# Performance work log

Hardware: AMD Instinct MI355X
Metric: run time of the kernel (lower is better)

The kernel has to match this reference:

```python
import jax, jax.numpy as jnp
import numpy as np
from jax import lax

DN = ('NCHW', 'OIHW', 'NCHW')
BN_EPS = 1e-5


def _avg_pool(x, k, stride):
    # PyTorch AvgPool2d with count_include_pad=True: divide by k*k always
    p = k // 2
    s = lax.reduce_window(x, 0.0, lax.add, (1, 1, k, k), (1, 1, stride, stride),
                          [(0, 0), (0, 0), (p, p), (p, p)])
    return s / float(k * k)


def setup_inputs() -> dict:
    key = jax.random.key(0)
    k0, k1, k2 = jax.random.split(key, 3)
    x = jax.random.normal(k0, (8, 3, 1024, 1024), jnp.float32)
    weight = jax.random.normal(k1, (1, 5), jnp.float32)          # nn.Parameter(1,5)
    conv_w = jax.random.normal(k2, (5, 3, 7, 7), jnp.float32) * 0.05
    bn_gamma = jnp.ones((5,), jnp.float32)
    bn_beta = jnp.zeros((5,), jnp.float32)
    bn_mean = jnp.zeros((5,), jnp.float32)
    bn_var = jnp.ones((5,), jnp.float32)
    return {"x": x, "weight": weight, "conv_w": conv_w,
            "bn_gamma": bn_gamma, "bn_beta": bn_beta,
            "bn_mean": bn_mean, "bn_var": bn_var}


def reference(x, weight, conv_w, bn_gamma, bn_beta, bn_mean, bn_var):
    # stage 1: 3x3 avgpool stride 2
    x = _avg_pool(x, 3, 2)                                  # [b,3,512,512]
    image_a = jnp.mean(x, axis=1, keepdims=True)            # [b,1,512,512]

    # attention branch: Conv(3->5,k7,s2,p3) + BN(eval) -> spatial mean -> tanh
    wa = lax.conv_general_dilated(x, conv_w, (2, 2), [(3, 3), (3, 3)],
                                  dimension_numbers=DN)     # [b,5,256,256]
    wa = (wa - bn_mean[None, :, None, None]) * (bn_gamma[None, :, None, None] /
          jnp.sqrt(bn_var[None, :, None, None] + BN_EPS)) + bn_beta[None, :, None, None]
    weight_att = jnp.tanh(jnp.mean(wa, axis=(2, 3)))        # [b,5]

    # Gaussian-Laplacian kernel from learned scalar GL
    GL = weight[0, 0]
    a1 = GL * 4.0
    a2 = -a1 / 8.0
    a3 = -a1 / 16.0
    ker = jnp.zeros((1, 1, 5, 5), jnp.float32)
    for r, c in [(0, 2), (1, 1), (1, 3), (2, 0), (2, 4), (3, 1), (3, 3), (4, 2)]:
        ker = ker.at[0, 0, r, c].set(a3)
    for r, c in [(1, 2), (2, 1), (2, 3), (3, 2)]:
        ker = ker.at[0, 0, r, c].set(a2)
    ker = ker.at[0, 0, 2, 2].set(a1)

    x_GL = lax.conv_general_dilated(image_a, ker, (1, 1), [(2, 2), (2, 2)],
                                    dimension_numbers=DN)   # [b,1,512,512]
    x_GL = jnp.abs(x_GL)
    x_GL = jnp.where(x_GL < 1e-6, 0.0, x_GL)                # zero tiny values (relu is no-op after abs)

    b, c, h, w = x_GL.shape
    t = x_GL.reshape(b, 1, h * w)                           # [b,1,N]
    x_GL_max = jnp.max(t, axis=-1)                          # [b,1]
    pos = t > 0
    all_sum = jnp.sum(pos, axis=-1)                         # [b,1]

    # 101 cubic-spaced bin edges in [0,10]
    xv = jnp.asarray(10.0 * (np.arange(101, dtype=np.float64) / 100.0) ** 3, jnp.float32)  # [101]
    sub_sum = jnp.sum(pos & (t <= xv[None, :, None]), axis=-1)  # [b,101]
    percentage = sub_sum.astype(jnp.float32) / all_sum.astype(jnp.float32)  # [b,101]

    # per-sample target percentiles (sorted)
    ps = jnp.stack([0.2 + 0.05 * weight_att[:, 1],
                    0.4 + 0.05 * weight_att[:, 2],
                    0.6 + 0.05 * weight_att[:, 3],
                    0.8 + 0.05 * weight_att[:, 4]])         # [4,b]
    thr_pct = jnp.sort(ps, axis=0).T                        # [b,4]

    z = jnp.abs(percentage[:, None, :] - thr_pct[:, :, None])  # [b,4,101]
    closest = jnp.argmin(z, axis=-1)                        # [b,4]
    threshold = xv[closest]                                 # [b,4]

    t_min = jnp.concatenate([jnp.zeros_like(x_GL_max), threshold], axis=-1)[:, :, None]  # [b,5,1]
    t_max = jnp.concatenate([threshold, x_GL_max], axis=-1)[:, :, None]                  # [b,5,1]
    mask = ((t > t_min) & (t <= t_max)).astype(jnp.float32).reshape(b, 5, h, w)

    # multi-stage 9x9 avg pooling
    m = _avg_pool(mask, 9, 1)
    m = _avg_pool(m, 9, 1)
    m = _avg_pool(m, 9, 2)                                  # [b,5,h//2,w//2]
    m = m.reshape(b, 5, -1)
    mn = jnp.min(m, axis=2, keepdims=True)
    mx = jnp.max(m, axis=2, keepdims=True)
    norm = (m - mn) / (mx - mn)
    return norm.reshape(b, 5, h // 2, w // 2)
```

## Files before the change

### kernel.cpp

```cpp
#include <hip/hip_runtime.h>
#include <math.h>

#pragma clang fp contract(off)

#define B 8
#define SP2 262144
#define SP3 65536

#define POOLF  4194304
#define MASKQF 6291456
#define TRIHF  10485760
#define TAILF  20971520

__global__ void k1_pool3(const float* __restrict__ x, double* __restrict__ imga,
                         double* __restrict__ rcs) {
    __shared__ double redE[2][3][128], redO[2][3][128];
    __shared__ double edge[2][3][5];
    int tid = threadIdx.x;
    int q = tid & 127;
    int r = tid >> 7;
    int rowIdx = blockIdx.x * 2 + r;
    int yo = rowIdx & 511;
    int b  = rowIdx >> 9;
    int xb = 8 * q;
    double pv[3][4];
    for (int c = 0; c < 3; ++c) {
        const float* p = x + ((size_t)(b * 3 + c)) * 1048576;
        double s0 = 0.0, s1 = 0.0, s2 = 0.0, s3 = 0.0;
        #pragma unroll
        for (int dy = 0; dy < 3; ++dy) {
            int iy = 2 * yo - 1 + dy;
            if ((unsigned)iy >= 1024u) continue;
            const float* row = p + (size_t)iy * 1024 + xb;
            float4 fM = *(const float4*)row;
            float4 fR = *(const float4*)(row + 4);
            float  vm1 = (q > 0) ? row[-1] : 0.f;
            s0 += (double)vm1  + (double)fM.x + (double)fM.y;
            s1 += (double)fM.y + (double)fM.z + (double)fM.w;
            s2 += (double)fM.w + (double)fR.x + (double)fR.y;
            s3 += (double)fR.y + (double)fR.z + (double)fR.w;
        }
        pv[c][0] = s0 * (1.0 / 9.0); pv[c][1] = s1 * (1.0 / 9.0);
        pv[c][2] = s2 * (1.0 / 9.0); pv[c][3] = s3 * (1.0 / 9.0);
        redE[r][c][q] = pv[c][0] + pv[c][2];
        redO[r][c][q] = pv[c][1] + pv[c][3];
        if (q == 0)   { edge[r][c][0] = pv[c][0]; edge[r][c][1] = pv[c][1]; }
        if (q == 127) { edge[r][c][2] = pv[c][1]; edge[r][c][3] = pv[c][2]; edge[r][c][4] = pv[c][3]; }
    }
    double* ia = imga + (size_t)b * SP2 + yo * 512 + 4 * q;
    #pragma unroll
    for (int k = 0; k < 4; ++k)
        ia[k] = ((pv[0][k] + pv[1][k]) + pv[2][k]) * (1.0 / 3.0);
    __syncthreads();
    for (int s = 64; s > 0; s >>= 1) {
        if (q < s) {
            #pragma unroll
            for (int c = 0; c < 3; ++c) {
                redE[r][c][q] += redE[r][c][q + s];
                redO[r][c][q] += redO[r][c][q + s];
            }
        }
        __syncthreads();
    }
    if (q < 21) {
        int c = q / 7, kx = q - c * 7;
        double E = redE[r][c][0], O = redO[r][c][0];
        double val;
        switch (kx) {
            case 0: val = O - edge[r][c][2] - edge[r][c][4]; break;
            case 1: val = E - edge[r][c][3]; break;
            case 2: val = O - edge[r][c][4]; break;
            case 3: val = E; break;
            case 4: val = O; break;
            case 5: val = E - edge[r][c][0]; break;
            default: val = O - edge[r][c][1]; break;
        }
        rcs[((size_t)(b * 3 + c) * 512 + yo) * 7 + kx] = val;
    }
}

__global__ void k2b(const double* __restrict__ rcs, const float* __restrict__ convw,
                    double* __restrict__ partial) {
    int b = blockIdx.x >> 2;
    int o = (blockIdx.x & 3) + 1;
    int t = threadIdx.x;
    double acc = 0.0;
    #pragma unroll 7
    for (int tap = 0; tap < 147; ++tap) {
        int c = tap / 49;
        int k = tap - c * 49;
        int ky = k / 7, kx = k - ky * 7;
        int iy = 2 * t + ky - 3;
        if ((unsigned)iy < 512u) {
            double w = (double)convw[o * 147 + tap];
            acc += w * rcs[((size_t)(b * 3 + c) * 512 + iy) * 7 + kx];
        }
    }
    __shared__ double red[256];
    red[t] = acc;
    __syncthreads();
    for (int s2 = 128; s2 > 0; s2 >>= 1) {
        if (t < s2) red[t] += red[t + s2];
        __syncthreads();
    }
    if (t == 0) partial[blockIdx.x] = red[0];
}

__global__ void k3_gl(const double* __restrict__ imga, const float* __restrict__ weight,
                      uchar4* __restrict__ codes) {
    __shared__ double xv[101];
    for (int i = threadIdx.x; i < 101; i += 256) {
        double d = (double)i / 100.0;
        xv[i] = (double)(float)(10.0 * d * d * d);
    }
    __syncthreads();
    int idx = blockIdx.x * 256 + threadIdx.x;
    int xo = idx & 511;
    int yo = (idx >> 9) & 511;
    int b  = idx >> 18;
    const double* im = imga + (size_t)b * SP2;
    double GL = (double)weight[0];
    double a1 = GL * 4.0, a2 = -a1 / 8.0, a3 = -a1 / 16.0;
    auto g = [&](int y, int x) -> double {
        if ((unsigned)y >= 512u || (unsigned)x >= 512u) return 0.0;
        return im[y * 512 + x];
    };
    double v = a1 * g(yo, xo)
             + a2 * (g(yo - 1, xo) + g(yo, xo - 1) + g(yo, xo + 1) + g(yo + 1, xo))
             + a3 * (g(yo - 2, xo) + g(yo - 1, xo - 1) + g(yo - 1, xo + 1) + g(yo, xo - 2)
                   + g(yo, xo + 2) + g(yo + 1, xo - 1) + g(yo + 1, xo + 1) + g(yo + 2, xo));
    double t = fabs(v);
    const double EPS = 6e-7;
    int cM;
    if (t < 1e-6) cM = 255;
    else if (t > xv[100]) cM = 101;
    else {
        int lo = 0, hi = 100;
        while (lo < hi) { int mid = (lo + hi) >> 1; if (t <= xv[mid]) hi = mid; else lo = mid + 1; }
        cM = lo;
    }
    double ua = t - EPS;
    int cA;
    if (ua < 1e-6) cA = 255;
    else if (ua > xv[100]) cA = 101;
    else {
        int k = (cM == 101) ? 100 : ((cM == 255) ? 100 : cM);
        while (k > 0 && ua <= xv[k - 1]) --k;
        cA = k;
    }
    double ub = t + EPS;
    int cB;
    if (ub < 1e-6) cB = 255;
    else if (ub > xv[100]) cB = 101;
    else {
        int k = (cM == 255) ? 0 : ((cM == 101) ? 100 : cM);
        while (k < 100 && ub > xv[k]) ++k;
        cB = k;
    }
    codes[idx] = make_uchar4((unsigned char)cM, (unsigned char)cA, (unsigned char)cB, 0);
}

__global__ void k4_hist(const uchar4* __restrict__ codes, int* __restrict__ ghist) {
    int b = blockIdx.y;
    __shared__ int h[102];
    for (int i = threadIdx.x; i < 102; i += 256) h[i] = 0;
    __syncthreads();
    const uchar4* cb = codes + (size_t)b * SP2;
    for (int p = blockIdx.x * 256 + threadIdx.x; p < SP2; p += 64 * 256) {
        int c = cb[p].x;
        if (c != 255) atomicAdd(&h[c], 1);
    }
    __syncthreads();
    for (int i = threadIdx.x; i < 102; i += 256)
        if (h[i]) atomicAdd(&ghist[b * 102 + i], h[i]);
}

__global__ void k5_thr(const int* __restrict__ ghist, const double* __restrict__ partial,
                       const float* __restrict__ bn_gamma, const float* __restrict__ bn_beta,
                       const float* __restrict__ bn_mean, const float* __restrict__ bn_var,
                       int* __restrict__ thrLo, int* __restrict__ thrHi) {
    int b = blockIdx.x;
    int t = threadIdx.x;
    __shared__ int    hS[102];
    __shared__ int    cumI[101];
    __shared__ double pct[101];
    __shared__ double ps[4];
    __shared__ int    allS;
    if (t < 102) hS[t] = ghist[b * 102 + t];
    __syncthreads();
    if (t == 0) {
        int all = 0;
        for (int k = 0; k < 102; ++k) all += hS[k];
        allS = all;
        int cum = 0;
        for (int k = 0; k < 101; ++k) { cum += hS[k]; cumI[k] = cum; }
    }
    __syncthreads();
    double alld = (double)allS;
    if (t < 101) pct[t] = (double)cumI[t] / alld;
    if (t < 4) {
        int o = t + 1;
        double s = partial[b * 4 + t];
        double m = s / 65536.0;
        double scale = (double)bn_gamma[o] / sqrt((double)bn_var[o] + 1e-5);
        double val = (m - (double)bn_mean[o]) * scale + (double)bn_beta[o];
        const double base[4] = {0.2, 0.4, 0.6, 0.8};
        ps[t] = base[t] + 0.05 * tanh(val);
    }
    __syncthreads();
    if (t == 0) {
        for (int i = 0; i < 4; ++i)
            for (int j = i + 1; j < 4; ++j)
                if (ps[j] < ps[i]) { double tp = ps[i]; ps[i] = ps[j]; ps[j] = tp; }
    }
    __syncthreads();
    if (t < 4) {
        const double EPS_TIE = 1.2e-7;
        double target = ps[t];
        double best = 1e300; int bi = 0;
        for (int k = 0; k < 101; ++k) {
            double z = fabs(pct[k] - target);
            if (z < best) { best = z; bi = k; }
        }
        int lo = bi, hi = bi;
        for (int k = 0; k < 101; ++k) {
            double z = fabs(pct[k] - target);
            if (z <= best + EPS_TIE) { if (k < lo) lo = k; if (k > hi) hi = k; }
        }
        int cnt = cumI[hi] - cumI[lo];
        if (cnt > 2) { lo = bi; hi = bi; }
        thrLo[b * 4 + t] = lo;
        thrHi[b * 4 + t] = hi;
    }
}

__global__ void k6_mask(const uchar4* __restrict__ codes, const int* __restrict__ thrLo,
                        const int* __restrict__ thrHi, unsigned char* __restrict__ mq) {
    int idx4 = blockIdx.x * 256 + threadIdx.x;
    int b  = idx4 >> 16;
    int sp0 = (idx4 & 65535) * 4;
    const uchar4* cb = codes + (size_t)b * SP2 + sp0;
    uchar4 cd[4] = {cb[0], cb[1], cb[2], cb[3]};
    const int* tL = thrLo + b * 4;
    const int* tH = thrHi + b * 4;
    int t0L = tL[0], t1L = tL[1], t2L = tL[2], t3L = tL[3];
    int t0H = tH[0], t1H = tH[1], t2H = tH[2], t3H = tH[3];
    unsigned char wv[5][4];
    #pragma unroll
    for (int px = 0; px < 4; ++px) {
        int w0 = 0, w1 = 0, w2 = 0, w3 = 0, w4 = 0;
        int cand[2] = {cd[px].y, cd[px].z};
        #pragma unroll
        for (int ci = 0; ci < 2; ++ci) {
            int c = cand[ci];
            if (c == 255) continue;
            if (c <= t0L) ++w0; else if (c <= t1L) ++w1; else if (c <= t2L) ++w2;
            else if (c <= t3L) ++w3; else ++w4;
            if (c <= t0H) ++w0; else if (c <= t1H) ++w1; else if (c <= t2H) ++w2;
            else if (c <= t3H) ++w3; else ++w4;
        }
        wv[0][px] = (unsigned char)w0; wv[1][px] = (unsigned char)w1;
        wv[2][px] = (unsigned char)w2; wv[3][px] = (unsigned char)w3;
        wv[4][px] = (unsigned char)w4;
    }
    unsigned char* mb = mq + (size_t)b * 5 * SP2 + sp0;
    #pragma unroll
    for (int pl = 0; pl < 5; ++pl)
        *(uchar4*)(mb + (size_t)pl * SP2) = make_uchar4(wv[pl][0], wv[pl][1], wv[pl][2], wv[pl][3]);
}

__global__ void __launch_bounds__(256) k7f(const unsigned char* __restrict__ mq,
                                           float* __restrict__ out,
                                           float* __restrict__ pmn, float* __restrict__ pmx) {
    __shared__ unsigned short shH[39][512];
    __shared__ unsigned short shB[31][512];
    __shared__ float smn[256], smx[256];
    unsigned short (*shT)[512] = shH;
    int (*shD)[256] = (int (*)[256])shB;

    int blk = (blockIdx.x & 7) * 160 + (blockIdx.x >> 3);
    int g  = blk & 31;
    int ch = blk >> 5;
    int y0 = g * 8;
    int tid = threadIdx.x;
    int lane = tid & 63;
    int rsel = tid >> 6;

    for (int it = 0; it < 10; ++it) {
        int rl = 4 * it + rsel;
        if (rl >= 39) break;
        int gr = 2 * y0 - 12 + rl;
        int x0 = lane * 8;
        uint4 pk = make_uint4(0u, 0u, 0u, 0u);
        if ((unsigned)gr < 512u) {
            const uint2* r8 = (const uint2*)(mq + (size_t)ch * SP2 + (size_t)gr * 512);
            uint2 cL = (lane > 0)  ? r8[lane - 1] : make_uint2(0u, 0u);
            uint2 cM = r8[lane];
            uint2 cR = (lane < 63) ? r8[lane + 1] : make_uint2(0u, 0u);
            int v[24];
            auto unpack = [](uint2 c, int* dst) {
                dst[0] = c.x & 255; dst[1] = (c.x >> 8) & 255; dst[2] = (c.x >> 16) & 255; dst[3] = (c.x >> 24) & 255;
                dst[4] = c.y & 255; dst[5] = (c.y >> 8) & 255; dst[6] = (c.y >> 16) & 255; dst[7] = (c.y >> 24) & 255;
            };
            unpack(cL, v); unpack(cM, v + 8); unpack(cR, v + 16);
            int bx[16];
            int s = 0;
            #pragma unroll
            for (int i = 0; i < 9; ++i) s += v[i];
            bx[0] = s;
            #pragma unroll
            for (int k = 1; k < 16; ++k) { s += v[k + 8] - v[k - 1]; bx[k] = s; }
            if (lane == 0)  { bx[0] = 0; bx[1] = 0; bx[2] = 0; bx[3] = 0; }
            if (lane == 63) { bx[12] = 0; bx[13] = 0; bx[14] = 0; bx[15] = 0; }
            int t = 0;
            #pragma unroll
            for (int i = 0; i < 9; ++i) t += bx[i];
            unsigned short o[8];
            o[0] = (unsigned short)t;
            #pragma unroll
            for (int i = 1; i < 8; ++i) { t += bx[i + 8] - bx[i - 1]; o[i] = (unsigned short)t; }
            pk.x = (unsigned)o[0] | ((unsigned)o[1] << 16);
            pk.y = (unsigned)o[2] | ((unsigned)o[3] << 16);
            pk.z = (unsigned)o[4] | ((unsigned)o[5] << 16);
            pk.w = (unsigned)o[6] | ((unsigned)o[7] << 16);
        }
        *(uint4*)&shH[rl][x0] = pk;
    }
    __syncthreads();

    #pragma unroll
    for (int half = 0; half < 2; ++half) {
        int x = tid + half * 256;
        int s = 0;
        #pragma unroll
        for (int i = 0; i < 9; ++i) s += (int)shH[i][x];
        int j0 = 2 * y0 - 8;
        shB[0][x] = (unsigned short)(((unsigned)j0 < 512u) ? s : 0);
        #pragma unroll
        for (int jl = 1; jl < 31; ++jl) {
            s += (int)shH[jl + 8][x] - (int)shH[jl - 1][x];
            int j = j0 + jl;
            shB[jl][x] = (unsigned short)(((unsigned)j < 512u) ? s : 0);
        }
    }
    __syncthreads();

    #pragma unroll
    for (int half = 0; half < 2; ++half) {
        int x = tid + half * 256;
        int s = 0;
        #pragma unroll
        for (int i = 0; i < 9; ++i) s += (int)shB[i][x];
        unsigned short tv[23];
        tv[0] = (unsigned short)s;
        #pragma unroll
        for (int rl = 1; rl < 23; ++rl) {
            s += (int)shB[rl + 8][x] - (int)shB[rl - 1][x];
            tv[rl] = (unsigned short)s;
        }
        __syncthreads();
        #pragma unroll
        for (int rl = 0; rl < 23; ++rl) shT[rl][x] = tv[rl];
        if (half == 0) __syncthreads();
    }
    __syncthreads();

    for (int it = 0; it < 6; ++it) {
        int rl = 4 * it + rsel;
        if (rl >= 23) break;
        int gr = 2 * y0 - 4 + rl;
        int ox0 = lane * 4;
        int o0 = 0, o1 = 0, o2 = 0, o3 = 0;
        if ((unsigned)gr < 512u) {
            int v[15];
            #pragma unroll
            for (int i = 0; i < 15; ++i) {
                int ix = 2 * ox0 - 4 + i;
                v[i] = ((unsigned)ix < 512u) ? (int)shT[rl][ix] : 0;
            }
            int s = 0;
            #pragma unroll
            for (int i = 0; i < 9; ++i) s += v[i];
            o0 = s;
            s += v[9] + v[10] - v[0] - v[1];   o1 = s;
            s += v[11] + v[12] - v[2] - v[3];  o2 = s;
            s += v[13] + v[14] - v[4] - v[5];  o3 = s;
        }
        shD[rl][ox0] = o0; shD[rl][ox0 + 1] = o1; shD[rl][ox0 + 2] = o2; shD[rl][ox0 + 3] = o3;
    }
    __syncthreads();

    int x = tid;
    float lmn = 3.4e38f, lmx = -3.4e38f;
    float* op = out + (size_t)ch * SP3 + (size_t)y0 * 256 + x;
    #pragma unroll
    for (int dy = 0; dy < 8; ++dy) {
        int s = 0;
        #pragma unroll
        for (int d = 0; d < 9; ++d) s += shD[2 * dy + d][x];
        float val = (float)s / 2125764.0f;
        op[(size_t)dy * 256] = val;
        lmn = fminf(lmn, val); lmx = fmaxf(lmx, val);
    }
    smn[tid] = lmn; smx[tid] = lmx;
    __syncthreads();
    for (int st = 128; st > 0; st >>= 1) {
        if (tid < st) {
            smn[tid] = fminf(smn[tid], smn[tid + st]);
            smx[tid] = fmaxf(smx[tid], smx[tid + st]);
        }
        __syncthreads();
    }
    if (tid == 0) { pmn[blk] = smn[0]; pmx[blk] = smx[0]; }
}

__global__ void k9_norm(float* __restrict__ o, const float* __restrict__ pmn,
                        const float* __restrict__ pmx) {
    __shared__ float sm[2];
    int idx = blockIdx.x * 256 + threadIdx.x;
    int ch = idx >> 16;
    int lane = threadIdx.x & 63;
    if (threadIdx.x < 64) {
        float v = (lane < 32) ? pmn[ch * 32 + lane] : pmx[ch * 32 + (lane - 32)];
        #pragma unroll
        for (int off = 16; off > 0; off >>= 1) {
            float u = __shfl_xor(v, off, 64);
            v = (lane < 32) ? fminf(v, u) : fmaxf(v, u);
        }
        if (lane == 0)  sm[0] = v;
        if (lane == 32) sm[1] = v;
    }
    __syncthreads();
    float a = sm[0];
    float bmax = sm[1];
    o[idx] = (o[idx] - a) / (bmax - a);
}

extern "C" void kernel_launch(void* const* d_in, const int* in_sizes, int n_in,
                              void* d_out, int out_size, void* d_ws, size_t ws_size,
                              hipStream_t stream) {
    const float* x      = (const float*)d_in[0];
    const float* weight = (const float*)d_in[1];
    const float* conv_w = (const float*)d_in[2];
    const float* bn_g   = (const float*)d_in[3];
    const float* bn_b   = (const float*)d_in[4];
    const float* bn_m   = (const float*)d_in[5];
    const float* bn_v   = (const float*)d_in[6];
    float* out = (float*)d_out;
    float* ws  = (float*)d_ws;

    double* imga   = (double*)ws;
    uchar4* codes  = (uchar4*)(ws + POOLF);
    unsigned char* maskq = (unsigned char*)(ws + MASKQF);
    double* rcs    = (double*)(ws + TRIHF);
    double* partial = (double*)(ws + TAILF);
    int*    thrLo   = (int*)(ws + TAILF + 4096);
    int*    thrHi   = thrLo + 32;
    int*    ghist   = thrHi + 32;
    float*  pmn     = (float*)(ghist + 816);
    float*  pmx     = pmn + 1280;

    hipMemsetAsync(ghist, 0, 816 * sizeof(int), stream);

    k1_pool3  <<<2048, 256, 0, stream>>>(x, imga, rcs);
    k2b       <<<32, 256, 0, stream>>>(rcs, conv_w, partial);
    k3_gl     <<<8192, 256, 0, stream>>>(imga, weight, codes);
    k4_hist   <<<dim3(64, B), 256, 0, stream>>>(codes, ghist);
    k5_thr    <<<B, 128, 0, stream>>>(ghist, partial, bn_g, bn_b, bn_m, bn_v, thrLo, thrHi);
    k6_mask   <<<2048, 256, 0, stream>>>(codes, thrLo, thrHi, maskq);
    k7f       <<<1280, 256, 0, stream>>>(maskq, out, pmn, pmx);
    k9_norm   <<<10240, 256, 0, stream>>>(out, pmn, pmx);
}
```

Measured before the change: 140.4 us.

## Fuse attention conv into threshold kernel, widen k7f blocks, vectorize histogram reads

Removes the separate k2b launch and computes the attention-branch conv sums inside the threshold kernel, now run with 256 threads per batch. This saves one launch but serialises four output channels within only 8 blocks. k4_hist now reads four codes per uint4 load. k7f runs 512 threads so each thread covers one column in the separable pooling passes, which also drops extra syncs. k1_pool3 remaps block indices to interleave batches across the grid.

```diff
diff --git a/kernel.cpp b/kernel.cpp
--- a/kernel.cpp
+++ b/kernel.cpp
@@ -16,10 +16,11 @@
                          double* __restrict__ rcs) {
     __shared__ double redE[2][3][128], redO[2][3][128];
     __shared__ double edge[2][3][5];
+    int blk = (blockIdx.x & 7) * 256 + (blockIdx.x >> 3);
     int tid = threadIdx.x;
     int q = tid & 127;
     int r = tid >> 7;
-    int rowIdx = blockIdx.x * 2 + r;
+    int rowIdx = blk * 2 + r;
     int yo = rowIdx & 511;
     int b  = rowIdx >> 9;
     int xb = 8 * q;
@@ -77,33 +78,6 @@
         }
         rcs[((size_t)(b * 3 + c) * 512 + yo) * 7 + kx] = val;
     }
-}
-
-__global__ void k2b(const double* __restrict__ rcs, const float* __restrict__ convw,
-                    double* __restrict__ partial) {
-    int b = blockIdx.x >> 2;
-    int o = (blockIdx.x & 3) + 1;
-    int t = threadIdx.x;
-    double acc = 0.0;
-    #pragma unroll 7
-    for (int tap = 0; tap < 147; ++tap) {
-        int c = tap / 49;
-        int k = tap - c * 49;
-        int ky = k / 7, kx = k - ky * 7;
-        int iy = 2 * t + ky - 3;
-        if ((unsigned)iy < 512u) {
-            double w = (double)convw[o * 147 + tap];
-            acc += w * rcs[((size_t)(b * 3 + c) * 512 + iy) * 7 + kx];
-        }
-    }
-    __shared__ double red[256];
-    red[t] = acc;
-    __syncthreads();
-    for (int s2 = 128; s2 > 0; s2 >>= 1) {
-        if (t < s2) red[t] += red[t + s2];
-        __syncthreads();
-    }
-    if (t == 0) partial[blockIdx.x] = red[0];
 }
 
 __global__ void k3_gl(const double* __restrict__ imga, const float* __restrict__ weight,
@@ -165,26 +139,61 @@
     __shared__ int h[102];
     for (int i = threadIdx.x; i < 102; i += 256) h[i] = 0;
     __syncthreads();
-    const uchar4* cb = codes + (size_t)b * SP2;
-    for (int p = blockIdx.x * 256 + threadIdx.x; p < SP2; p += 64 * 256) {
-        int c = cb[p].x;
-        if (c != 255) atomicAdd(&h[c], 1);
+    const uint4* cb = (const uint4*)(codes + (size_t)b * SP2);
+    for (int p = blockIdx.x * 256 + threadIdx.x; p < SP2 / 4; p += 64 * 256) {
+        uint4 v = cb[p];
+        int c0 = v.x & 255, c1 = v.y & 255, c2 = v.z & 255, c3 = v.w & 255;
+        if (c0 != 255) atomicAdd(&h[c0], 1);
+        if (c1 != 255) atomicAdd(&h[c1], 1);
+        if (c2 != 255) atomicAdd(&h[c2], 1);
+        if (c3 != 255) atomicAdd(&h[c3], 1);
     }
     __syncthreads();
     for (int i = threadIdx.x; i < 102; i += 256)
         if (h[i]) atomicAdd(&ghist[b * 102 + i], h[i]);
 }
 
-__global__ void k5_thr(const int* __restrict__ ghist, const double* __restrict__ partial,
-                       const float* __restrict__ bn_gamma, const float* __restrict__ bn_beta,
-                       const float* __restrict__ bn_mean, const float* __restrict__ bn_var,
-                       int* __restrict__ thrLo, int* __restrict__ thrHi) {
+__global__ void k25_thr(const double* __restrict__ rcs, const float* __restrict__ convw,
+                        const int* __restrict__ ghist,
+                        const float* __restrict__ bn_gamma, const float* __restrict__ bn_beta,
+                        const float* __restrict__ bn_mean, const float* __restrict__ bn_var,
+                        int* __restrict__ thrLo, int* __restrict__ thrHi) {
     int b = blockIdx.x;
     int t = threadIdx.x;
+    __shared__ double red[256];
+    __shared__ double ps[4];
+    for (int oi = 0; oi < 4; ++oi) {
+        int o = oi + 1;
+        double acc = 0.0;
+        #pragma unroll 7
+        for (int tap = 0; tap < 147; ++tap) {
+            int c = tap / 49;
+            int k = tap - c * 49;
+            int ky = k / 7, kx = k - ky * 7;
+            int iy = 2 * t + ky - 3;
+            if ((unsigned)iy < 512u) {
+                double w = (double)convw[o * 147 + tap];
+                acc += w * rcs[((size_t)(b * 3 + c) * 512 + iy) * 7 + kx];
+            }
+        }
+        red[t] = acc;
+        __syncthreads();
+        for (int s2 = 128; s2 > 0; s2 >>= 1) {
+            if (t < s2) red[t] += red[t + s2];
+            __syncthreads();
+        }
+        if (t == 0) {
+            double m = red[0] / 65536.0;
+            double scale = (double)bn_gamma[o] / sqrt((double)bn_var[o] + 1e-5);
+            double val = (m - (double)bn_mean[o]) * scale + (double)bn_beta[o];
+            const double base[4] = {0.2, 0.4, 0.6, 0.8};
+            ps[oi] = base[oi] + 0.05 * tanh(val);
+        }
+        __syncthreads();
+    }
     __shared__ int    hS[102];
     __shared__ int    cumI[101];
     __shared__ double pct[101];
-    __shared__ double ps[4];
     __shared__ int    allS;
     if (t < 102) hS[t] = ghist[b * 102 + t];
     __syncthreads();
@@ -194,25 +203,13 @@
         allS = all;
         int cum = 0;
         for (int k = 0; k < 101; ++k) { cum += hS[k]; cumI[k] = cum; }
-    }
-    __syncthreads();
-    double alld = (double)allS;
-    if (t < 101) pct[t] = (double)cumI[t] / alld;
-    if (t < 4) {
-        int o = t + 1;
-        double s = partial[b * 4 + t];
-        double m = s / 65536.0;
-        double scale = (double)bn_gamma[o] / sqrt((double)bn_var[o] + 1e-5);
-        double val = (m - (double)bn_mean[o]) * scale + (double)bn_beta[o];
-        const double base[4] = {0.2, 0.4, 0.6, 0.8};
-        ps[t] = base[t] + 0.05 * tanh(val);
-    }
-    __syncthreads();
-    if (t == 0) {
         for (int i = 0; i < 4; ++i)
             for (int j = i + 1; j < 4; ++j)
                 if (ps[j] < ps[i]) { double tp = ps[i]; ps[i] = ps[j]; ps[j] = tp; }
     }
+    __syncthreads();
+    double alld = (double)allS;
+    if (t < 101) pct[t] = (double)cumI[t] / alld;
     __syncthreads();
     if (t < 4) {
         const double EPS_TIE = 1.2e-7;
@@ -269,12 +266,12 @@
         *(uchar4*)(mb + (size_t)pl * SP2) = make_uchar4(wv[pl][0], wv[pl][1], wv[pl][2], wv[pl][3]);
 }
 
-__global__ void __launch_bounds__(256) k7f(const unsigned char* __restrict__ mq,
+__global__ void __launch_bounds__(512) k7f(const unsigned char* __restrict__ mq,
                                            float* __restrict__ out,
                                            float* __restrict__ pmn, float* __restrict__ pmx) {
     __shared__ unsigned short shH[39][512];
     __shared__ unsigned short shB[31][512];
-    __shared__ float smn[256], smx[256];
+    __shared__ float smn[512], smx[512];
     unsigned short (*shT)[512] = shH;
     int (*shD)[256] = (int (*)[256])shB;
 
@@ -286,8 +283,8 @@
     int lane = tid & 63;
     int rsel = tid >> 6;
 
-    for (int it = 0; it < 10; ++it) {
-        int rl = 4 * it + rsel;
+    for (int it = 0; it < 5; ++it) {
+        int rl = 8 * it + rsel;
         if (rl >= 39) break;
         int gr = 2 * y0 - 12 + rl;
         int x0 = lane * 8;
@@ -328,26 +325,27 @@
     }
     __syncthreads();
 
-    #pragma unroll
-    for (int half = 0; half < 2; ++half) {
-        int x = tid + half * 256;
+    {
+        int x = tid;
         int s = 0;
         #pragma unroll
         for (int i = 0; i < 9; ++i) s += (int)shH[i][x];
         int j0 = 2 * y0 - 8;
-        shB[0][x] = (unsigned short)(((unsigned)j0 < 512u) ? s : 0);
+        unsigned short bv[31];
+        bv[0] = (unsigned short)(((unsigned)j0 < 512u) ? s : 0);
         #pragma unroll
         for (int jl = 1; jl < 31; ++jl) {
             s += (int)shH[jl + 8][x] - (int)shH[jl - 1][x];
             int j = j0 + jl;
-            shB[jl][x] = (unsigned short)(((unsigned)j < 512u) ? s : 0);
-        }
-    }
-    __syncthreads();
-
-    #pragma unroll
-    for (int half = 0; half < 2; ++half) {
-        int x = tid + half * 256;
+            bv[jl] = (unsigned short)(((unsigned)j < 512u) ? s : 0);
+        }
+        #pragma unroll
+        for (int jl = 0; jl < 31; ++jl) shB[jl][x] = bv[jl];
+    }
+    __syncthreads();
+
+    {
+        int x = tid;
         int s = 0;
         #pragma unroll
         for (int i = 0; i < 9; ++i) s += (int)shB[i][x];
@@ -358,15 +356,13 @@
             s += (int)shB[rl + 8][x] - (int)shB[rl - 1][x];
             tv[rl] = (unsigned short)s;
         }
-        __syncthreads();
         #pragma unroll
         for (int rl = 0; rl < 23; ++rl) shT[rl][x] = tv[rl];
-        if (half == 0) __syncthreads();
-    }
-    __syncthreads();
-
-    for (int it = 0; it < 6; ++it) {
-        int rl = 4 * it + rsel;
+    }
+    __syncthreads();
+
+    for (int it = 0; it < 3; ++it) {
+        int rl = 8 * it + rsel;
         if (rl >= 23) break;
         int gr = 2 * y0 - 4 + rl;
         int ox0 = lane * 4;
@@ -390,11 +386,13 @@
     }
     __syncthreads();
 
-    int x = tid;
+    int x = tid & 255;
+    int dy0 = (tid >> 8) * 4;
     float lmn = 3.4e38f, lmx = -3.4e38f;
     float* op = out + (size_t)ch * SP3 + (size_t)y0 * 256 + x;
     #pragma unroll
-    for (int dy = 0; dy < 8; ++dy) {
+    for (int k = 0; k < 4; ++k) {
+        int dy = dy0 + k;
         int s = 0;
         #pragma unroll
         for (int d = 0; d < 9; ++d) s += shD[2 * dy + d][x];
@@ -404,7 +402,7 @@
     }
     smn[tid] = lmn; smx[tid] = lmx;
     __syncthreads();
-    for (int st = 128; st > 0; st >>= 1) {
+    for (int st = 256; st > 0; st >>= 1) {
         if (tid < st) {
             smn[tid] = fminf(smn[tid], smn[tid + st]);
             smx[tid] = fmaxf(smx[tid], smx[tid + st]);
@@ -453,8 +451,7 @@
     uchar4* codes  = (uchar4*)(ws + POOLF);
     unsigned char* maskq = (unsigned char*)(ws + MASKQF);
     double* rcs    = (double*)(ws + TRIHF);
-    double* partial = (double*)(ws + TAILF);
-    int*    thrLo   = (int*)(ws + TAILF + 4096);
+    int*    thrLo   = (int*)(ws + TAILF);
     int*    thrHi   = thrLo + 32;
     int*    ghist   = thrHi + 32;
     float*  pmn     = (float*)(ghist + 816);
@@ -463,11 +460,10 @@
     hipMemsetAsync(ghist, 0, 816 * sizeof(int), stream);
 
     k1_pool3  <<<2048, 256, 0, stream>>>(x, imga, rcs);
-    k2b       <<<32, 256, 0, stream>>>(rcs, conv_w, partial);
     k3_gl     <<<8192, 256, 0, stream>>>(imga, weight, codes);
     k4_hist   <<<dim3(64, B), 256, 0, stream>>>(codes, ghist);
-    k5_thr    <<<B, 128, 0, stream>>>(ghist, partial, bn_g, bn_b, bn_m, bn_v, thrLo, thrHi);
+    k25_thr   <<<B, 256, 0, stream>>>(rcs, conv_w, ghist, bn_g, bn_b, bn_m, bn_v, thrLo, thrHi);
     k6_mask   <<<2048, 256, 0, stream>>>(codes, thrLo, thrHi, maskq);
-    k7f       <<<1280, 256, 0, stream>>>(maskq, out, pmn, pmx);
+    k7f       <<<1280, 512, 0, stream>>>(maskq, out, pmn, pmx);
     k9_norm   <<<10240, 256, 0, stream>>>(out, pmn, pmx);
 }
```

Result: slower. 209.4 us (+49.2%).
